# Performance work log

Measured on AMD Instinct MI355X. Metric: run time of the kernel, lower is better.

The kernel has to match this reference:

```python
import jax, jax.numpy as jnp
import numpy as np

N_HEAD, D_MODEL, D_HEAD = 16, 1024, 64
SEQ, BATCH = 1024, 8
SCALE = 1.0 / (D_HEAD ** 0.5)
LN_EPS = 1e-5


def setup_inputs() -> dict:
    key = jax.random.key(0)
    ks = jax.random.split(key, 16)
    dk = N_HEAD * D_HEAD  # == D_MODEL
    init_qkv = 1.0 / np.sqrt(D_MODEL)
    init_out = 1.0 / np.sqrt(dk)
    u = lambda k, shp, lo, hi: jax.random.uniform(k, shp, jnp.float32, lo, hi)
    inp = {
        'dec_inp': jax.random.normal(ks[0], (SEQ, BATCH, D_MODEL), jnp.float32),
        'attn_mask': jnp.triu(jnp.ones((SEQ, SEQ), dtype=bool), k=1),  # causal
        'query_mean': u(ks[1], (dk, D_MODEL), -init_qkv, init_qkv),
        'key_mean': u(ks[2], (dk, D_MODEL), -init_qkv, init_qkv),
        'value_mean': u(ks[3], (dk, D_MODEL), -init_qkv, init_qkv),
        'query_std': u(ks[4], (dk, D_MODEL), 2 * np.log(init_qkv), np.log(init_qkv)),
        'key_std': u(ks[5], (dk, D_MODEL), 2 * np.log(init_qkv), np.log(init_qkv)),
        'value_std': u(ks[6], (dk, D_MODEL), 2 * np.log(init_qkv), np.log(init_qkv)),
        'output_mean': u(ks[7], (D_MODEL, dk), -init_out, init_out),
        'output_std': u(ks[8], (D_MODEL, dk), 2 * np.log(init_out), np.log(init_out)),
        'ln_gamma': jnp.ones((D_MODEL,), jnp.float32),
        'ln_beta': jnp.zeros((D_MODEL,), jnp.float32),
        # per-forward reparameterization noise (training mode)
        'eps_q': jax.random.normal(ks[9], (dk, D_MODEL), jnp.float32),
        'eps_k': jax.random.normal(ks[10], (dk, D_MODEL), jnp.float32),
        'eps_v': jax.random.normal(ks[11], (dk, D_MODEL), jnp.float32),
        'eps_o': jax.random.normal(ks[12], (D_MODEL, dk), jnp.float32),
    }
    return inp


def _forward(dec_inp, query_mean, key_mean, value_mean, query_std, key_std,
             value_std, output_mean, output_std, ln_gamma, ln_beta,
             eps_q, eps_k, eps_v, eps_o, attn_mask):
    S, B, _ = dec_inp.shape
    # Bayesian weight sampling: w = mean + eps * exp(std)
    qw = query_mean + eps_q * jnp.exp(query_std)
    kw = key_mean + eps_k * jnp.exp(key_std)
    vw = value_mean + eps_v * jnp.exp(value_std)
    # NOTE: original code (bug kept for faithfulness) builds the output weight
    # from value_mean + output_diff, not output_mean.
    ow = value_mean + eps_o * jnp.exp(output_std)

    head_q = (dec_inp @ qw.T).reshape(S, B, N_HEAD, D_HEAD)
    head_k = (dec_inp @ kw.T).reshape(S, B, N_HEAD, D_HEAD)
    head_v = (dec_inp @ vw.T).reshape(S, B, N_HEAD, D_HEAD)

    score = jnp.einsum('ibnd,jbnd->ijbn', head_q, head_k) * SCALE
    score = jnp.where(attn_mask[:, :, None, None], -jnp.inf, score)
    prob = jax.nn.softmax(score, axis=1)  # softmax over j (key) axis
    attn_vec = jnp.einsum('ijbn,jbnd->ibnd', prob, head_v).reshape(S, B, N_HEAD * D_HEAD)

    attn_out = attn_vec @ ow.T
    x = dec_inp + attn_out
    mu = jnp.mean(x, axis=-1, keepdims=True)
    var = jnp.var(x, axis=-1, keepdims=True)
    output = (x - mu) * jax.lax.rsqrt(var + LN_EPS) * ln_gamma + ln_beta

    theta_mean = jnp.concatenate([query_mean, key_mean, value_mean, output_mean.T], -1)
    theta_std = jnp.concatenate([query_std, key_std, value_std, output_std.T], -1)
    kl = jnp.mean(theta_mean ** 2 - theta_std * 2.0 + jnp.exp(theta_std * 2.0)) / 2.0
    return output, kl


def reference(dec_inp, attn_mask, query_mean, key_mean, value_mean, query_std,
              key_std, value_std, output_mean, output_std, ln_gamma, ln_beta,
              eps_q, eps_k, eps_v, eps_o):
    return _forward(dec_inp, query_mean, key_mean, value_mean, query_std,
                    key_std, value_std, output_mean, output_std, ln_gamma,
                    ln_beta, eps_q, eps_k, eps_v, eps_o, attn_mask)
```

## Files before the change

kernel.cpp:

```cpp
#include <hip/hip_runtime.h>

typedef _Float16 f16x8 __attribute__((ext_vector_type(8)));
typedef _Float16 f16x4 __attribute__((ext_vector_type(4)));
typedef float    f32x4 __attribute__((ext_vector_type(4)));

static __device__ __forceinline__ f32x4 mfma16(f16x8 a, f16x8 b, f32x4 c) {
    return __builtin_amdgcn_mfma_f32_16x16x32_f16(a, b, c, 0, 0, 0);
}

static __device__ __forceinline__ void gload_lds16(const _Float16* g, _Float16* lds) {
    __builtin_amdgcn_global_load_lds(
        (const __attribute__((address_space(1))) unsigned int*)g,
        (__attribute__((address_space(3))) unsigned int*)lds, 16, 0, 0);
}

__global__ __launch_bounds__(256) void k_prep(
    const float* __restrict__ qm, const float* __restrict__ km, const float* __restrict__ vm,
    const float* __restrict__ qs, const float* __restrict__ ks, const float* __restrict__ vs,
    const float* __restrict__ om, const float* __restrict__ os,
    const float* __restrict__ eq, const float* __restrict__ ek,
    const float* __restrict__ ev, const float* __restrict__ eo,
    _Float16* __restrict__ wq, _Float16* __restrict__ wk,
    _Float16* __restrict__ wv, _Float16* __restrict__ wo,
    float* __restrict__ part,
    const float* __restrict__ dec, _Float16* __restrict__ xh)
{
    if (blockIdx.x >= 1024) {
        int i = ((blockIdx.x - 1024) * 256 + threadIdx.x) * 4;
        float4 v = *(const float4*)&dec[i];
        f16x4 hv;
        hv[0] = (_Float16)v.x; hv[1] = (_Float16)v.y;
        hv[2] = (_Float16)v.z; hv[3] = (_Float16)v.w;
        *(f16x4*)&xh[i] = hv;
        return;
    }
    int i = (blockIdx.x * 256 + threadIdx.x) * 4;
    f32x4 aqm = *(const f32x4*)&qm[i], akm = *(const f32x4*)&km[i], avm = *(const f32x4*)&vm[i];
    f32x4 aqs = *(const f32x4*)&qs[i], aks = *(const f32x4*)&ks[i], avs = *(const f32x4*)&vs[i];
    f32x4 aom = *(const f32x4*)&om[i], aos = *(const f32x4*)&os[i];
    f32x4 veq = *(const f32x4*)&eq[i], vek = *(const f32x4*)&ek[i];
    f32x4 vev = *(const f32x4*)&ev[i], veo = *(const f32x4*)&eo[i];
    f16x4 hq, hk, hv, ho;
    float t = 0.f;
    #pragma unroll
    for (int j = 0; j < 4; ++j) {
        hq[j] = (_Float16)(aqm[j] + veq[j] * __expf(aqs[j]));
        hk[j] = (_Float16)(akm[j] + vek[j] * __expf(aks[j]));
        hv[j] = (_Float16)(avm[j] + vev[j] * __expf(avs[j]));
        ho[j] = (_Float16)(avm[j] + veo[j] * __expf(aos[j]));
        t += aqm[j]*aqm[j] - 2.f*aqs[j] + __expf(2.f*aqs[j])
           + akm[j]*akm[j] - 2.f*aks[j] + __expf(2.f*aks[j])
           + avm[j]*avm[j] - 2.f*avs[j] + __expf(2.f*avs[j])
           + aom[j]*aom[j] - 2.f*aos[j] + __expf(2.f*aos[j]);
    }
    *(f16x4*)&wq[i] = hq;
    *(f16x4*)&wk[i] = hk;
    *(f16x4*)&wv[i] = hv;
    *(f16x4*)&wo[i] = ho;
    #pragma unroll
    for (int m = 1; m < 64; m <<= 1) t += __shfl_xor(t, m, 64);
    __shared__ float red[4];
    int w = threadIdx.x >> 6, lane = threadIdx.x & 63;
    if (lane == 0) red[w] = t;
    __syncthreads();
    if (threadIdx.x == 0) part[blockIdx.x] = red[0] + red[1] + red[2] + red[3];
}

__global__ __launch_bounds__(256) void k_gemm(
    const _Float16* __restrict__ A, const _Float16* __restrict__ B0,
    _Float16* __restrict__ C0, const float* __restrict__ resid,
    float* __restrict__ xout, int mode)
{
    __shared__ __align__(16) _Float16 As[128 * 64];
    __shared__ __align__(16) _Float16 Bs[128 * 64];
    const int K = 1024, N = 1024;
    const _Float16* Bp = B0 + (size_t)blockIdx.z * 1048576u;
    _Float16* Cp = C0 + (size_t)blockIdx.z * 8388608u;
    int flat = blockIdx.y * 8 + blockIdx.x;
    int xcd = flat & 7, j = flat >> 3;
    int tM = (xcd * 8 + (j & 7)) * 128;
    int tN = (j >> 3) * 128;
    int tid = threadIdx.x, w = tid >> 6, lane = tid & 63;
    int wm = w & 1, wn = w >> 1;
    int q = lane >> 4, r = lane & 15;
    int csrc = ((lane & 7) ^ (lane >> 3)) * 8;
    int srow = lane >> 3;
    f32x4 acc[4][4] = {};
    for (int kk = 0; kk < K; kk += 64) {
        __syncthreads();
        #pragma unroll
        for (int i = 0; i < 4; ++i) {
            int chunk = w * 4 + i;
            int row = chunk * 8 + srow;
            gload_lds16(A  + (size_t)(tM + row) * K + kk + csrc, &As[chunk * 512]);
            gload_lds16(Bp + (size_t)(tN + row) * K + kk + csrc, &Bs[chunk * 512]);
        }
        __syncthreads();
        #pragma unroll
        for (int kc = 0; kc < 2; ++kc) {
            f16x8 af[4], bf[4];
            #pragma unroll
            for (int m = 0; m < 4; ++m) {
                int row = wm*64 + m*16 + r;
                int pos = ((kc*4 + q) ^ (r & 7)) * 8;
                af[m] = *(const f16x8*)&As[row*64 + pos];
            }
            #pragma unroll
            for (int n = 0; n < 4; ++n) {
                int row = wn*64 + n*16 + r;
                int pos = ((kc*4 + q) ^ (r & 7)) * 8;
                bf[n] = *(const f16x8*)&Bs[row*64 + pos];
            }
            #pragma unroll
            for (int m = 0; m < 4; ++m)
                #pragma unroll
                for (int n = 0; n < 4; ++n)
                    acc[m][n] = mfma16(af[m], bf[n], acc[m][n]);
        }
    }
    float sc = (mode == 0 && blockIdx.z == 0) ? 0.125f : 1.0f;
    #pragma unroll
    for (int m = 0; m < 4; ++m)
      #pragma unroll
      for (int n = 0; n < 4; ++n)
        #pragma unroll
        for (int t = 0; t < 4; ++t) {
            int row = tM + wm*64 + m*16 + q*4 + t;
            int col = tN + wn*64 + n*16 + r;
            size_t o = (size_t)row * N + col;
            if (mode == 0) Cp[o] = (_Float16)(acc[m][n][t] * sc);
            else           xout[o] = resid[o] + acc[m][n][t];
        }
}

__global__ __launch_bounds__(256) void k_vtrans(const _Float16* __restrict__ V,
                                                _Float16* __restrict__ Vt)
{
    __shared__ __align__(16) _Float16 L[64 * 72];
    int c = blockIdx.x;
    int b = c >> 4, h = c & 15;
    int s0 = blockIdx.y * 64;
    int tid = threadIdx.x;
    #pragma unroll
    for (int rep = 0; rep < 2; ++rep) {
        int idx = rep * 256 + tid;
        int sl = idx >> 3, ch = idx & 7;
        f16x8 v = *(const f16x8*)&V[((size_t)(s0 + sl) * 8 + b) * 1024 + h * 64 + ch * 8];
        *(f16x8*)&L[sl * 72 + ch * 8] = v;
    }
    __syncthreads();
    #pragma unroll
    for (int rep = 0; rep < 2; ++rep) {
        int idx = rep * 256 + tid;
        int d = idx >> 3, c2 = idx & 7;
        f16x8 o;
        #pragma unroll
        for (int e = 0; e < 8; ++e) o[e] = L[(c2 * 8 + e) * 72 + d];
        *(f16x8*)&Vt[((size_t)c * 64 + d) * 1024 + s0 + c2 * 8] = o;
    }
}

__global__ __launch_bounds__(256, 3) void k_attn(
    const _Float16* __restrict__ Qb, const _Float16* __restrict__ Kb,
    const _Float16* __restrict__ Vtg, _Float16* __restrict__ AVo)
{
    __shared__ __align__(16) _Float16 Ks[2][64 * 64];
    __shared__ __align__(16) _Float16 Vs[2][64 * 64];
    __shared__ __align__(16) _Float16 Ps[4 * 32 * 72];
    const int bh = blockIdx.x;
    const int b = bh & 7, h = bh >> 3;
    const int cbh = b * 16 + h;
    const int qt = (0x15623740u >> (blockIdx.y * 4)) & 7;
    const int tid = threadIdx.x, w = tid >> 6, lane = tid & 63;
    const int q = lane >> 4, r = lane & 15;
    const int i0 = qt * 128 + w * 32;
    const int csrc = ((lane & 7) ^ (lane >> 3)) * 8;
    const int srow = lane >> 3;

    f16x8 qf[2][2];
    #pragma unroll
    for (int it = 0; it < 2; ++it)
      #pragma unroll
      for (int kc = 0; kc < 2; ++kc)
        qf[it][kc] = *(const f16x8*)&Qb[((size_t)(i0 + it*16 + r)*8 + b)*1024 + h*64 + kc*32 + q*8];

    f32x4 ot[4][2] = {};
    float mrun[2] = {-1e30f, -1e30f}, lrun[2] = {0.f, 0.f};
    _Float16* Pw = &Ps[w * 2304];

    auto stage = [&](int kt, int buf) __attribute__((always_inline)) {
        #pragma unroll
        for (int ii = 0; ii < 2; ++ii) {
            int chunk = w * 2 + ii;
            int row = chunk * 8 + srow;
            gload_lds16(Kb  + ((size_t)(kt*64 + row)*8 + b)*1024 + h*64 + csrc, &Ks[buf][chunk*512]);
            gload_lds16(Vtg + ((size_t)(cbh*64 + row))*1024 + kt*64 + csrc,     &Vs[buf][chunk*512]);
        }
    };

    auto tile = [&](int kt, int buf, bool MASK) __attribute__((always_inline)) {
        f32x4 st[4][2] = {};
        #pragma unroll
        for (int kc = 0; kc < 2; ++kc) {
            f16x8 kf[4];
            #pragma unroll
            for (int jt = 0; jt < 4; ++jt) {
                int pos = ((kc*4 + q) ^ (r & 7)) * 8;
                kf[jt] = *(const f16x8*)&Ks[buf][(jt*16 + r)*64 + pos];
            }
            #pragma unroll
            for (int jt = 0; jt < 4; ++jt)
              #pragma unroll
              for (int it = 0; it < 2; ++it)
                st[jt][it] = mfma16(kf[jt], qf[it][kc], st[jt][it]);
        }

        #pragma unroll
        for (int it = 0; it < 2; ++it) {
            if (MASK) {
                int il = i0 + it*16 + r;
                #pragma unroll
                for (int jt = 0; jt < 4; ++jt)
                  #pragma unroll
                  for (int t = 0; t < 4; ++t)
                    if (kt*64 + jt*16 + q*4 + t > il) st[jt][it][t] = -1e30f;
            }
            float mx = -1e30f;
            #pragma unroll
            for (int jt = 0; jt < 4; ++jt) {
                f32x4 s4 = st[jt][it];
                mx = fmaxf(mx, fmaxf(fmaxf(s4[0], s4[1]), fmaxf(s4[2], s4[3])));
            }
            mx = fmaxf(mx, __shfl_xor(mx, 16, 64));
            mx = fmaxf(mx, __shfl_xor(mx, 32, 64));
            float mnew = fmaxf(mrun[it], mx);
            float al = __expf(mrun[it] - mnew);
            mrun[it] = mnew;
            float ps = 0.f;
            #pragma unroll
            for (int jt = 0; jt < 4; ++jt) {
                f16x4 hv;
                #pragma unroll
                for (int t = 0; t < 4; ++t) {
                    float e = __expf(st[jt][it][t] - mnew);
                    ps += e;
                    hv[t] = (_Float16)e;
                }
                *(f16x4*)&Pw[(it*16 + r)*72 + jt*16 + q*4] = hv;
            }
            ps += __shfl_xor(ps, 16, 64);
            ps += __shfl_xor(ps, 32, 64);
            lrun[it] = lrun[it] * al + ps;
            #pragma unroll
            for (int dtb = 0; dtb < 4; ++dtb) ot[dtb][it] *= al;
        }

        #pragma unroll
        for (int kc = 0; kc < 2; ++kc) {
            f16x8 vf[4], pf[2];
            #pragma unroll
            for (int dtb = 0; dtb < 4; ++dtb) {
                int pos = ((kc*4 + q) ^ (r & 7)) * 8;
                vf[dtb] = *(const f16x8*)&Vs[buf][(dtb*16 + r)*64 + pos];
            }
            #pragma unroll
            for (int it = 0; it < 2; ++it)
                pf[it] = *(const f16x8*)&Pw[(it*16 + r)*72 + kc*32 + q*8];
            #pragma unroll
            for (int dtb = 0; dtb < 4; ++dtb)
              #pragma unroll
              for (int it = 0; it < 2; ++it)
                ot[dtb][it] = mfma16(vf[dtb], pf[it], ot[dtb][it]);
        }
    };

    stage(0, 0);
    __syncthreads();
    for (int kt = 0; kt < 2*qt; ++kt) {
        stage(kt + 1, (kt + 1) & 1);
        tile(kt, kt & 1, false);
        __syncthreads();
    }
    {
        int kt = 2*qt;
        stage(kt + 1, (kt + 1) & 1);
        tile(kt, kt & 1, true);
        __syncthreads();
        tile(kt + 1, (kt + 1) & 1, true);
    }

    #pragma unroll
    for (int it = 0; it < 2; ++it) {
        float inv = 1.f / lrun[it];
        int s = i0 + it*16 + r;
        #pragma unroll
        for (int dtb = 0; dtb < 4; ++dtb) {
            f16x4 hv;
            #pragma unroll
            for (int t = 0; t < 4; ++t) hv[t] = (_Float16)(ot[dtb][it][t] * inv);
            *(f16x4*)&AVo[((size_t)s*8 + b)*1024 + h*64 + dtb*16 + q*4] = hv;
        }
    }
}

__global__ __launch_bounds__(256) void k_ln(float* __restrict__ x,
    const float* __restrict__ g, const float* __restrict__ bta,
    const float* __restrict__ part)
{
    __shared__ float rs[4], rs2[4];
    int w = threadIdx.x >> 6, lane = threadIdx.x & 63;
    if (blockIdx.x == 8192) {
        float s = 0.f;
        for (int i = threadIdx.x; i < 1024; i += 256) s += part[i];
        #pragma unroll
        for (int m = 1; m < 64; m <<= 1) s += __shfl_xor(s, m, 64);
        if (lane == 0) rs[w] = s;
        __syncthreads();
        if (threadIdx.x == 0)
            x[8388608] = (rs[0] + rs[1] + rs[2] + rs[3]) * (0.5f / 4194304.f);
        return;
    }
    int row = blockIdx.x;
    float* xr = x + (size_t)row * 1024;
    int t4 = threadIdx.x * 4;
    float4 v = *(const float4*)&xr[t4];
    float s  = v.x + v.y + v.z + v.w;
    float s2 = v.x*v.x + v.y*v.y + v.z*v.z + v.w*v.w;
    #pragma unroll
    for (int m = 1; m < 64; m <<= 1) { s += __shfl_xor(s, m, 64); s2 += __shfl_xor(s2, m, 64); }
    if (lane == 0) { rs[w] = s; rs2[w] = s2; }
    __syncthreads();
    s  = rs[0] + rs[1] + rs[2] + rs[3];
    s2 = rs2[0] + rs2[1] + rs2[2] + rs2[3];
    float mu = s * (1.f / 1024.f);
    float var = s2 * (1.f / 1024.f) - mu * mu;
    float rstd = rsqrtf(var + 1e-5f);
    float4 gv = *(const float4*)&g[t4];
    float4 bv = *(const float4*)&bta[t4];
    float4 ov;
    ov.x = (v.x - mu) * rstd * gv.x + bv.x;
    ov.y = (v.y - mu) * rstd * gv.y + bv.y;
    ov.z = (v.z - mu) * rstd * gv.z + bv.z;
    ov.w = (v.w - mu) * rstd * gv.w + bv.w;
    *(float4*)&xr[t4] = ov;
}

extern "C" void kernel_launch(void* const* d_in, const int* in_sizes, int n_in,
                              void* d_out, int out_size, void* d_ws, size_t ws_size,
                              hipStream_t stream)
{
    (void)in_sizes; (void)n_in; (void)out_size; (void)ws_size;
    const float* dec   = (const float*)d_in[0];
    const float* qm    = (const float*)d_in[2];
    const float* km    = (const float*)d_in[3];
    const float* vm    = (const float*)d_in[4];
    const float* qs    = (const float*)d_in[5];
    const float* ks    = (const float*)d_in[6];
    const float* vs    = (const float*)d_in[7];
    const float* om    = (const float*)d_in[8];
    const float* os    = (const float*)d_in[9];
    const float* gamma = (const float*)d_in[10];
    const float* beta  = (const float*)d_in[11];
    const float* eq    = (const float*)d_in[12];
    const float* ek    = (const float*)d_in[13];
    const float* ev    = (const float*)d_in[14];
    const float* eo    = (const float*)d_in[15];

    char* ws = (char*)d_ws;
    _Float16* WQ   = (_Float16*)ws;
    float*    PART = (float*)(ws + (8ull  << 20));
    _Float16* XH   = (_Float16*)(ws + (9ull  << 20));
    _Float16* Qh   = (_Float16*)(ws + (25ull << 20));
    _Float16* Kh   = Qh + 8388608;
    _Float16* Vh   = Qh + 16777216;
    _Float16* Vtg  = XH;
    _Float16* AV   = Vh;
    float*    out  = (float*)d_out;

    k_prep<<<dim3(9216), dim3(256), 0, stream>>>(
        qm, km, vm, qs, ks, vs, om, os, eq, ek, ev, eo,
        WQ, WQ + 1048576, WQ + 2097152, WQ + 3145728, PART, dec, XH);
    k_gemm<<<dim3(8, 64, 3), dim3(256), 0, stream>>>(XH, WQ, Qh, dec, out, 0);
    k_vtrans<<<dim3(128, 16), dim3(256), 0, stream>>>(Vh, Vtg);
    k_attn<<<dim3(128, 8), dim3(256), 0, stream>>>(Qh, Kh, Vtg, AV);
    k_gemm<<<dim3(8, 64, 1), dim3(256), 0, stream>>>(AV, WQ + 3145728, Qh, dec, out, 1);
    k_ln<<<dim3(8193), dim3(256), 0, stream>>>(out, gamma, beta, PART);
}
```

Measured before the change: 308.4 us.

## Double-buffer GEMM LDS tiles with 256x128 blocks of eight waves

The projection GEMM now uses a 256x128 output tile computed by 8 waves (512 threads), with double-buffered LDS stages so the global-to-LDS load of the next K slice overlaps the MFMA work on the current one. Explicit barriers, waitcnts, sched_barriers and setprio control the interleaving, and the launch grids are halved to match. The aim is to hide global load latency and raise reuse of the B tile, at the cost of twice the LDS (96KB per block) and more complex synchronisation.

```diff
diff --git a/kernel.cpp b/kernel.cpp
--- a/kernel.cpp
+++ b/kernel.cpp
@@ -66,58 +66,85 @@
     if (threadIdx.x == 0) part[blockIdx.x] = red[0] + red[1] + red[2] + red[3];
 }
 
-__global__ __launch_bounds__(256) void k_gemm(
+__global__ __launch_bounds__(512, 2) void k_gemm(
     const _Float16* __restrict__ A, const _Float16* __restrict__ B0,
     _Float16* __restrict__ C0, const float* __restrict__ resid,
     float* __restrict__ xout, int mode)
 {
-    __shared__ __align__(16) _Float16 As[128 * 64];
-    __shared__ __align__(16) _Float16 Bs[128 * 64];
+    __shared__ __align__(16) _Float16 As[2][256 * 64];
+    __shared__ __align__(16) _Float16 Bs[2][128 * 64];
     const int K = 1024, N = 1024;
     const _Float16* Bp = B0 + (size_t)blockIdx.z * 1048576u;
     _Float16* Cp = C0 + (size_t)blockIdx.z * 8388608u;
+
     int flat = blockIdx.y * 8 + blockIdx.x;
     int xcd = flat & 7, j = flat >> 3;
-    int tM = (xcd * 8 + (j & 7)) * 128;
-    int tN = (j >> 3) * 128;
+    int tM = (xcd * 4 + (j & 3)) * 256;
+    int tN = (j >> 2) * 128;
+
     int tid = threadIdx.x, w = tid >> 6, lane = tid & 63;
-    int wm = w & 1, wn = w >> 1;
+    int wm = w >> 1, wn = w & 1;
     int q = lane >> 4, r = lane & 15;
-    int csrc = ((lane & 7) ^ (lane >> 3)) * 8;
     int srow = lane >> 3;
-    f32x4 acc[4][4] = {};
-    for (int kk = 0; kk < K; kk += 64) {
-        __syncthreads();
+    int csrc = ((lane & 7) ^ srow) * 8;
+
+    auto stage = [&](int t, int buf) __attribute__((always_inline)) {
+        int kk = t * 64;
         #pragma unroll
         for (int i = 0; i < 4; ++i) {
             int chunk = w * 4 + i;
-            int row = chunk * 8 + srow;
-            gload_lds16(A  + (size_t)(tM + row) * K + kk + csrc, &As[chunk * 512]);
-            gload_lds16(Bp + (size_t)(tN + row) * K + kk + csrc, &Bs[chunk * 512]);
-        }
-        __syncthreads();
+            gload_lds16(A + (size_t)(tM + chunk * 8 + srow) * K + kk + csrc,
+                        &As[buf][chunk * 512]);
+        }
+        #pragma unroll
+        for (int i = 0; i < 2; ++i) {
+            int chunk = w * 2 + i;
+            gload_lds16(Bp + (size_t)(tN + chunk * 8 + srow) * K + kk + csrc,
+                        &Bs[buf][chunk * 512]);
+        }
+    };
+
+    f32x4 acc[4][4] = {};
+
+    stage(0, 0);
+    asm volatile("s_waitcnt vmcnt(0)" ::: "memory");
+    __builtin_amdgcn_s_barrier();
+    stage(1, 1);
+
+    #pragma unroll 2
+    for (int t = 0; t < 16; ++t) {
+        const int cur = t & 1;
         #pragma unroll
         for (int kc = 0; kc < 2; ++kc) {
+            int pos = ((kc * 4 + q) ^ (r & 7)) * 8;
             f16x8 af[4], bf[4];
             #pragma unroll
-            for (int m = 0; m < 4; ++m) {
-                int row = wm*64 + m*16 + r;
-                int pos = ((kc*4 + q) ^ (r & 7)) * 8;
-                af[m] = *(const f16x8*)&As[row*64 + pos];
-            }
-            #pragma unroll
-            for (int n = 0; n < 4; ++n) {
-                int row = wn*64 + n*16 + r;
-                int pos = ((kc*4 + q) ^ (r & 7)) * 8;
-                bf[n] = *(const f16x8*)&Bs[row*64 + pos];
-            }
+            for (int m = 0; m < 4; ++m)
+                af[m] = *(const f16x8*)&As[cur][(wm * 64 + m * 16 + r) * 64 + pos];
+            #pragma unroll
+            for (int n = 0; n < 4; ++n)
+                bf[n] = *(const f16x8*)&Bs[cur][(wn * 64 + n * 16 + r) * 64 + pos];
+            __builtin_amdgcn_s_barrier();
+            asm volatile("s_waitcnt lgkmcnt(0)" ::: "memory");
+            __builtin_amdgcn_sched_barrier(0);
+            __builtin_amdgcn_s_setprio(1);
             #pragma unroll
             for (int m = 0; m < 4; ++m)
                 #pragma unroll
                 for (int n = 0; n < 4; ++n)
                     acc[m][n] = mfma16(af[m], bf[n], acc[m][n]);
-        }
-    }
+            __builtin_amdgcn_s_setprio(0);
+            __builtin_amdgcn_sched_barrier(0);
+            if (kc == 0) {
+                __builtin_amdgcn_s_barrier();
+            } else {
+                asm volatile("s_waitcnt vmcnt(0)" ::: "memory");
+                __builtin_amdgcn_s_barrier();
+            }
+        }
+        if (t < 14) stage(t + 2, cur);
+    }
+
     float sc = (mode == 0 && blockIdx.z == 0) ? 0.125f : 1.0f;
     #pragma unroll
     for (int m = 0; m < 4; ++m)
@@ -380,9 +407,9 @@
     k_prep<<<dim3(9216), dim3(256), 0, stream>>>(
         qm, km, vm, qs, ks, vs, om, os, eq, ek, ev, eo,
         WQ, WQ + 1048576, WQ + 2097152, WQ + 3145728, PART, dec, XH);
-    k_gemm<<<dim3(8, 64, 3), dim3(256), 0, stream>>>(XH, WQ, Qh, dec, out, 0);
+    k_gemm<<<dim3(8, 32, 3), dim3(512), 0, stream>>>(XH, WQ, Qh, dec, out, 0);
     k_vtrans<<<dim3(128, 16), dim3(256), 0, stream>>>(Vh, Vtg);
     k_attn<<<dim3(128, 8), dim3(256), 0, stream>>>(Qh, Kh, Vtg, AV);
-    k_gemm<<<dim3(8, 64, 1), dim3(256), 0, stream>>>(AV, WQ + 3145728, Qh, dec, out, 1);
+    k_gemm<<<dim3(8, 32, 1), dim3(512), 0, stream>>>(AV, WQ + 3145728, Qh, dec, out, 1);
     k_ln<<<dim3(8193), dim3(256), 0, stream>>>(out, gamma, beta, PART);
 }
```

Measured after the change: 321.8 us. 1.04x slower.
